# Kernel optimization log

Measured on AMD Instinct MI355X. Metric: run time of the kernel, lower is better.

Reference implementation:

```python
import jax, jax.numpy as jnp
import numpy as np

NUM_HEADS = 16
NUM_KV_HEADS = 4
HEAD_DIM = 128
BATCH = 4
SEQ = 2048  # equal per-sequence length; cu_seqlens = arange(BATCH+1)*SEQ


def setup_inputs() -> dict:
    key = jax.random.key(0)
    k1, k2, k3 = jax.random.split(key, 3)
    T = BATCH * SEQ
    q = jax.random.normal(k1, (T, NUM_HEADS * HEAD_DIM), dtype=jnp.float32)
    k = jax.random.normal(k2, (T, NUM_KV_HEADS * HEAD_DIM), dtype=jnp.float32)
    v = jax.random.normal(k3, (T, NUM_KV_HEADS * HEAD_DIM), dtype=jnp.float32)
    cu = jnp.arange(BATCH + 1, dtype=jnp.int32) * SEQ
    return {"q": q, "k": k, "v": v, "cu_seqlens_q": cu, "cu_seqlens_k": cu}


def reference(q, k, v, cu_seqlens_q, cu_seqlens_k):
    # Prefill varlen causal attention with GQA (block_tables=None path).
    # Sequences have equal length, so the ragged batch reshapes to dense [B,S,...].
    B = cu_seqlens_q.shape[0] - 1
    T = q.shape[0]
    S = T // B
    D = HEAD_DIM
    G = NUM_HEADS // NUM_KV_HEADS  # GQA group size
    qh = q.reshape(B, S, NUM_KV_HEADS, G, D)
    kh = k.reshape(B, S, NUM_KV_HEADS, D)
    vh = v.reshape(B, S, NUM_KV_HEADS, D)
    scale = 1.0 / np.sqrt(D).astype(np.float32)  # SDPA scale=None default
    # scores: [B, Hkv, G, Sq, Sk]
    scores = jnp.einsum('bqhgd,bkhd->bhgqk', qh, kh) * scale
    causal = jnp.tril(jnp.ones((S, S), dtype=bool))
    scores = jnp.where(causal, scores, jnp.finfo(scores.dtype).min)
    probs = jax.nn.softmax(scores, axis=-1)
    o = jnp.einsum('bhgqk,bkhd->bqhgd', probs, vh)
    return o.reshape(T, NUM_HEADS * HEAD_DIM)
```

## Files before the change

kernel.cpp:

```cpp
#include <hip/hip_runtime.h>


typedef __attribute__((ext_vector_type(8))) short bs8;
typedef __attribute__((ext_vector_type(16))) float f16x;
typedef __attribute__((ext_vector_type(4))) unsigned int u32x4;
typedef __attribute__((ext_vector_type(4))) unsigned short u16x4;
typedef unsigned short u16;
typedef unsigned int u32;

#define B_ 4
#define S_ 2048
#define HQ_ 16
#define HKV_ 4
#define NQT 16
#define NKT_TOT 32
#define TILE_ELEMS 8192

__device__ __forceinline__ u16 f2bf(float f) {
  u32 u = __float_as_uint(f);
  u += 0x7fffu + ((u >> 16) & 1u);
  return (u16)(u >> 16);
}

__global__ void pack_k(const float* __restrict__ k, u16* __restrict__ kp) {
  int g = blockIdx.x * 256 + threadIdx.x;
  int row = g >> 7;
  int col = (g & 127) << 2;
  int h = col >> 7, d0 = col & 127;
  int b = row >> 11, s = row & 2047;
  int kt = s >> 6, kv = s & 63;
  float4 vv = *(const float4*)(k + (size_t)row * 512 + col);
  int ti = (b * HKV_ + h) * NKT_TOT + kt;
  int e = kv * 128 + (d0 ^ (8 * (kv & 15)));
  u16x4 o;
  o.x = f2bf(vv.x); o.y = f2bf(vv.y); o.z = f2bf(vv.z); o.w = f2bf(vv.w);
  *(u16x4*)(kp + (size_t)ti * TILE_ELEMS + e) = o;
}

__global__ void pack_v(const float* __restrict__ v, u16* __restrict__ vp) {
  __shared__ u16 img[TILE_ELEMS];
  int ti = blockIdx.x;
  int kt = ti & 31;
  int bh = ti >> 5;
  int h = bh & 3, b = bh >> 2;
  int t = threadIdx.x;
#pragma unroll
  for (int p = 0; p < 8; ++p) {
    int t2 = p * 256 + t;
    int kvr = t2 >> 5;
    int d0 = (t2 & 31) << 2;
    float4 vv = *(const float4*)(v + (size_t)(b * S_ + kt * 64 + kvr) * 512 + h * 128 + d0);
    float a[4] = {vv.x, vv.y, vv.z, vv.w};
#pragma unroll
    for (int j = 0; j < 4; ++j) {
      int d = d0 + j;
      img[(d >> 1) * 128 + (d & 1) * 64 + (kvr ^ (8 * ((d >> 1) & 7)))] = f2bf(a[j]);
    }
  }
  __syncthreads();
#pragma unroll
  for (int p = 0; p < 4; ++p) {
    int e0 = (p * 256 + t) * 8;
    *(bs8*)(vp + (size_t)ti * TILE_ELEMS + e0) = *(const bs8*)&img[e0];
  }
}

__device__ __forceinline__ void gl2lds(const u16* g, u16* l) {
  __builtin_amdgcn_global_load_lds((const __attribute__((address_space(1))) void*)g,
                                   (__attribute__((address_space(3))) void*)l,
                                   16, 0, 0);
}

__global__ __launch_bounds__(256, 2) void attn_fwd(
    const float* __restrict__ q, const u16* __restrict__ kp,
    const u16* __restrict__ vp, float* __restrict__ out) {
  __shared__ u16 Ks[2][TILE_ELEMS];
  __shared__ u16 Vs[2][TILE_ELEMS];

  const int bx = blockIdx.x;
  const int qt = (NQT - 1) - (bx >> 6);
  const int bh = bx & 63;
  const int b = bh >> 4, hq = bh & 15, hkv = hq >> 2;
  const int w = threadIdx.x >> 6, lane = threadIdx.x & 63;
  const int l31 = lane & 31, hi = lane >> 5;
  const int q0 = qt * 128;
  const float scale = 0.08838834764831845f;

  bs8 qf[8];
  {
    int row = b * S_ + q0 + w * 32 + l31;
    const float* qrow = q + (size_t)row * 2048 + hq * 128;
#pragma unroll
    for (int ki = 0; ki < 8; ++ki) {
      const float* p0 = qrow + ki * 16 + hi * 8;
      float4 a = *(const float4*)p0;
      float4 c = *(const float4*)(p0 + 4);
      bs8 f;
      f[0] = (short)f2bf(a.x * scale); f[1] = (short)f2bf(a.y * scale);
      f[2] = (short)f2bf(a.z * scale); f[3] = (short)f2bf(a.w * scale);
      f[4] = (short)f2bf(c.x * scale); f[5] = (short)f2bf(c.y * scale);
      f[6] = (short)f2bf(c.z * scale); f[7] = (short)f2bf(c.w * scale);
      qf[ki] = f;
    }
  }

  f16x O[4];
#pragma unroll
  for (int dt = 0; dt < 4; ++dt)
#pragma unroll
    for (int e = 0; e < 16; ++e) O[dt][e] = 0.f;
  float m_run = -1e30f, l_run = 0.f;

  const size_t tbase = (size_t)((b * HKV_ + hkv) * NKT_TOT) * TILE_ELEMS;
  const u16* kbase = kp + tbase;
  const u16* vbase = vp + tbase;
  const int nkt = 2 * qt + 2;
  const int myrowmax = q0 + w * 32 + 31;
  const int qpos = q0 + w * 32 + l31;

  const int swzk = 8 * (l31 & 15);
  const int swzv = 8 * ((l31 >> 1) & 7);
  const int vrowbase = (l31 >> 1) * 128 + (l31 & 1) * 64;

#pragma unroll
  for (int j = 0; j < 4; ++j) {
    int c = w * 4 + j;
    gl2lds(kbase + c * 512 + lane * 8, &Ks[0][c * 512]);
    gl2lds(vbase + c * 512 + lane * 8, &Vs[0][c * 512]);
  }
  asm volatile("s_waitcnt vmcnt(0)" ::: "memory");
  __syncthreads();

  int cur = 0;
  for (int kt = 0; kt < nkt; ++kt) {
    if (kt + 1 < nkt) {
      const u16* kg = kbase + (size_t)(kt + 1) * TILE_ELEMS;
      const u16* vg = vbase + (size_t)(kt + 1) * TILE_ELEMS;
#pragma unroll
      for (int j = 0; j < 4; ++j) {
        int c = w * 4 + j;
        gl2lds(kg + c * 512 + lane * 8, &Ks[cur ^ 1][c * 512]);
        gl2lds(vg + c * 512 + lane * 8, &Vs[cur ^ 1][c * 512]);
      }
    }

    if (kt * 64 <= myrowmax) {
      f16x Sa[2];
#pragma unroll
      for (int kb = 0; kb < 2; ++kb)
#pragma unroll
        for (int e = 0; e < 16; ++e) Sa[kb][e] = 0.f;

      __builtin_amdgcn_s_setprio(1);
#pragma unroll
      for (int ki = 0; ki < 8; ++ki) {
        int koff = (ki * 16 + hi * 8) ^ swzk;
#pragma unroll
        for (int kb = 0; kb < 2; ++kb) {
          bs8 kf = *(const bs8*)&Ks[cur][(kb * 32 + l31) * 128 + koff];
          Sa[kb] = __builtin_amdgcn_mfma_f32_32x32x16_bf16(kf, qf[ki], Sa[kb], 0, 0, 0);
        }
      }
      __builtin_amdgcn_s_setprio(0);

      if (kt >= 2 * qt) {
#pragma unroll
        for (int kb = 0; kb < 2; ++kb)
#pragma unroll
          for (int r = 0; r < 16; ++r) {
            int kvpos = kt * 64 + kb * 32 + (r & 3) + 8 * (r >> 2) + 4 * hi;
            if (kvpos > qpos) Sa[kb][r] = -1e30f;
          }
      }

      float pmax = Sa[0][0];
#pragma unroll
      for (int kb = 0; kb < 2; ++kb)
#pragma unroll
        for (int r = 0; r < 16; ++r) pmax = fmaxf(pmax, Sa[kb][r]);
      pmax = fmaxf(pmax, __shfl_xor(pmax, 32, 64));

      if (__any(pmax > m_run + 8.0f)) {
        float mnew = fmaxf(m_run, pmax);
        float alpha = __expf(m_run - mnew);
        m_run = mnew;
        l_run *= alpha;
#pragma unroll
        for (int r = 0; r < 16; ++r) {
          float ar = __shfl(alpha, (r & 3) + 8 * (r >> 2) + 4 * hi, 64);
#pragma unroll
          for (int dt = 0; dt < 4; ++dt) O[dt][r] *= ar;
        }
      }

      float psum = 0.f;
#pragma unroll
      for (int kb = 0; kb < 2; ++kb)
#pragma unroll
        for (int r = 0; r < 16; ++r) {
          float p = __expf(Sa[kb][r] - m_run);
          Sa[kb][r] = p;
          psum += p;
        }
      l_run += psum;

      bs8 pf[2][2];
#pragma unroll
      for (int kb = 0; kb < 2; ++kb) {
        u32 pk_[8];
#pragma unroll
        for (int j = 0; j < 8; ++j) {
          float lo = Sa[kb][2 * j], hif = Sa[kb][2 * j + 1];
          asm("v_cvt_pk_bf16_f32 %0, %1, %2" : "=v"(pk_[j]) : "v"(lo), "v"(hif));
        }
#pragma unroll
        for (int ks = 0; ks < 2; ++ks) {
          auto s0 = __builtin_amdgcn_permlane32_swap((int)pk_[4 * ks], (int)pk_[4 * ks + 2], false, false);
          auto s1 = __builtin_amdgcn_permlane32_swap((int)pk_[4 * ks + 1], (int)pk_[4 * ks + 3], false, false);
          u32x4 fw;
          fw[0] = (u32)s0[0]; fw[1] = (u32)s1[0]; fw[2] = (u32)s0[1]; fw[3] = (u32)s1[1];
          pf[kb][ks] = __builtin_bit_cast(bs8, fw);
        }
      }

      __builtin_amdgcn_s_setprio(1);
#pragma unroll
      for (int dt = 0; dt < 4; ++dt) {
#pragma unroll
        for (int kb = 0; kb < 2; ++kb)
#pragma unroll
          for (int ks = 0; ks < 2; ++ks) {
            int kvoff = (kb * 32 + ks * 16 + hi * 8) ^ swzv;
            bs8 vb = *(const bs8*)&Vs[cur][dt * 2048 + vrowbase + kvoff];
            O[dt] = __builtin_amdgcn_mfma_f32_32x32x16_bf16(pf[kb][ks], vb, O[dt], 0, 0, 0);
          }
      }
      __builtin_amdgcn_s_setprio(0);
    }

    asm volatile("s_waitcnt vmcnt(0)" ::: "memory");
    __syncthreads();
    cur ^= 1;
  }

  float lt = l_run + __shfl_xor(l_run, 32, 64);
  float inv = 1.0f / lt;
  const int orow0 = b * S_ + q0 + w * 32;
#pragma unroll
  for (int r = 0; r < 16; ++r) {
    int qr = (r & 3) + 8 * (r >> 2) + 4 * hi;
    float li = __shfl(inv, qr, 64);
    float* op = out + (size_t)(orow0 + qr) * 2048 + hq * 128 + l31;
#pragma unroll
    for (int dt = 0; dt < 4; ++dt) op[dt * 32] = O[dt][r] * li;
  }
}

extern "C" void kernel_launch(void* const* d_in, const int* in_sizes, int n_in,
                              void* d_out, int out_size, void* d_ws, size_t ws_size,
                              hipStream_t stream) {
  const float* q = (const float*)d_in[0];
  const float* k = (const float*)d_in[1];
  const float* v = (const float*)d_in[2];
  float* out = (float*)d_out;
  u16* kp = (u16*)d_ws;
  u16* vp = kp + (size_t)B_ * HKV_ * NKT_TOT * TILE_ELEMS;

  pack_k<<<(B_ * S_ * 512 / 4) / 256, 256, 0, stream>>>(k, kp);
  pack_v<<<B_ * HKV_ * NKT_TOT, 256, 0, stream>>>(v, vp);
  attn_fwd<<<B_ * HQ_ * NQT, 256, 0, stream>>>(q, kp, vp, out);
}
```

Measured before the change: 107.9 us.

## Software-pipeline QK^T of next tile with PV of current tile, use exp2

Restructures the main loop so the QK^T MFMAs for tile t+1 are interleaved with the PV MFMAs for tile t. K is staged two tiles ahead and V one tile ahead, so softmax work can overlap with matrix-core work. It folds log2(e) into the Q scale so exp2f replaces __expf, and uses tree reductions for the row max and row sum to shorten dependency chains. The cost is more live registers (Sa kept across iterations) and a more intricate buffer-slot schedule, which could hurt occupancy at 2 blocks per CU.

```diff
diff --git a/kernel.cpp b/kernel.cpp
--- a/kernel.cpp
+++ b/kernel.cpp
@@ -84,7 +84,7 @@
   const int w = threadIdx.x >> 6, lane = threadIdx.x & 63;
   const int l31 = lane & 31, hi = lane >> 5;
   const int q0 = qt * 128;
-  const float scale = 0.08838834764831845f;
+  const float scale2 = 0.08838834764831845f * 1.4426950408889634f;
 
   bs8 qf[8];
   {
@@ -96,10 +96,10 @@
       float4 a = *(const float4*)p0;
       float4 c = *(const float4*)(p0 + 4);
       bs8 f;
-      f[0] = (short)f2bf(a.x * scale); f[1] = (short)f2bf(a.y * scale);
-      f[2] = (short)f2bf(a.z * scale); f[3] = (short)f2bf(a.w * scale);
-      f[4] = (short)f2bf(c.x * scale); f[5] = (short)f2bf(c.y * scale);
-      f[6] = (short)f2bf(c.z * scale); f[7] = (short)f2bf(c.w * scale);
+      f[0] = (short)f2bf(a.x * scale2); f[1] = (short)f2bf(a.y * scale2);
+      f[2] = (short)f2bf(a.z * scale2); f[3] = (short)f2bf(a.w * scale2);
+      f[4] = (short)f2bf(c.x * scale2); f[5] = (short)f2bf(c.y * scale2);
+      f[6] = (short)f2bf(c.z * scale2); f[7] = (short)f2bf(c.w * scale2);
       qf[ki] = f;
     }
   }
@@ -109,80 +109,86 @@
   for (int dt = 0; dt < 4; ++dt)
 #pragma unroll
     for (int e = 0; e < 16; ++e) O[dt][e] = 0.f;
+  f16x Sa[2];
   float m_run = -1e30f, l_run = 0.f;
 
   const size_t tbase = (size_t)((b * HKV_ + hkv) * NKT_TOT) * TILE_ELEMS;
   const u16* kbase = kp + tbase;
   const u16* vbase = vp + tbase;
   const int nkt = 2 * qt + 2;
-  const int myrowmax = q0 + w * 32 + 31;
+  const int L = 2 * qt + (w >> 1);
   const int qpos = q0 + w * 32 + l31;
 
   const int swzk = 8 * (l31 & 15);
   const int swzv = 8 * ((l31 >> 1) & 7);
   const int vrowbase = (l31 >> 1) * 128 + (l31 & 1) * 64;
 
-#pragma unroll
-  for (int j = 0; j < 4; ++j) {
-    int c = w * 4 + j;
-    gl2lds(kbase + c * 512 + lane * 8, &Ks[0][c * 512]);
-    gl2lds(vbase + c * 512 + lane * 8, &Vs[0][c * 512]);
-  }
+#define STAGE_K(t_, slot_)                                              \
+  {                                                                     \
+    const u16* g_ = kbase + (size_t)(t_)*TILE_ELEMS;                    \
+    _Pragma("unroll") for (int j = 0; j < 4; ++j) {                     \
+      int c = w * 4 + j;                                                \
+      gl2lds(g_ + c * 512 + lane * 8, &Ks[slot_][c * 512]);             \
+    }                                                                   \
+  }
+#define STAGE_V(t_, slot_)                                              \
+  {                                                                     \
+    const u16* g_ = vbase + (size_t)(t_)*TILE_ELEMS;                    \
+    _Pragma("unroll") for (int j = 0; j < 4; ++j) {                     \
+      int c = w * 4 + j;                                                \
+      gl2lds(g_ + c * 512 + lane * 8, &Vs[slot_][c * 512]);             \
+    }                                                                   \
+  }
+
+  STAGE_K(0, 0);
+  STAGE_V(0, 0);
+  STAGE_K(1, 1);
   asm volatile("s_waitcnt vmcnt(0)" ::: "memory");
   __syncthreads();
 
-  int cur = 0;
-  for (int kt = 0; kt < nkt; ++kt) {
-    if (kt + 1 < nkt) {
-      const u16* kg = kbase + (size_t)(kt + 1) * TILE_ELEMS;
-      const u16* vg = vbase + (size_t)(kt + 1) * TILE_ELEMS;
-#pragma unroll
-      for (int j = 0; j < 4; ++j) {
-        int c = w * 4 + j;
-        gl2lds(kg + c * 512 + lane * 8, &Ks[cur ^ 1][c * 512]);
-        gl2lds(vg + c * 512 + lane * 8, &Vs[cur ^ 1][c * 512]);
-      }
-    }
-
-    if (kt * 64 <= myrowmax) {
-      f16x Sa[2];
-#pragma unroll
-      for (int kb = 0; kb < 2; ++kb)
-#pragma unroll
-        for (int e = 0; e < 16; ++e) Sa[kb][e] = 0.f;
-
-      __builtin_amdgcn_s_setprio(1);
-#pragma unroll
-      for (int ki = 0; ki < 8; ++ki) {
-        int koff = (ki * 16 + hi * 8) ^ swzk;
-#pragma unroll
-        for (int kb = 0; kb < 2; ++kb) {
-          bs8 kf = *(const bs8*)&Ks[cur][(kb * 32 + l31) * 128 + koff];
-          Sa[kb] = __builtin_amdgcn_mfma_f32_32x32x16_bf16(kf, qf[ki], Sa[kb], 0, 0, 0);
-        }
-      }
-      __builtin_amdgcn_s_setprio(0);
-
-      if (kt >= 2 * qt) {
+#pragma unroll
+  for (int kb = 0; kb < 2; ++kb)
+#pragma unroll
+    for (int e = 0; e < 16; ++e) Sa[kb][e] = 0.f;
+#pragma unroll
+  for (int ki = 0; ki < 8; ++ki) {
+    int koff = (ki * 16 + hi * 8) ^ swzk;
+#pragma unroll
+    for (int kb = 0; kb < 2; ++kb) {
+      bs8 kf = *(const bs8*)&Ks[0][(kb * 32 + l31) * 128 + koff];
+      Sa[kb] = __builtin_amdgcn_mfma_f32_32x32x16_bf16(kf, qf[ki], Sa[kb], 0, 0, 0);
+    }
+  }
+  __syncthreads();
+
+  for (int t = 0; t < nkt; ++t) {
+    if (t + 2 < nkt) STAGE_K(t + 2, t & 1);
+    if (t + 1 < nkt) STAGE_V(t + 1, (t + 1) & 1);
+
+    bs8 pf[2][2];
+    if (t <= L) {
+      if (t >= 2 * qt) {
 #pragma unroll
         for (int kb = 0; kb < 2; ++kb)
 #pragma unroll
           for (int r = 0; r < 16; ++r) {
-            int kvpos = kt * 64 + kb * 32 + (r & 3) + 8 * (r >> 2) + 4 * hi;
+            int kvpos = t * 64 + kb * 32 + (r & 3) + 8 * (r >> 2) + 4 * hi;
             if (kvpos > qpos) Sa[kb][r] = -1e30f;
           }
       }
-
-      float pmax = Sa[0][0];
-#pragma unroll
-      for (int kb = 0; kb < 2; ++kb)
-#pragma unroll
-        for (int r = 0; r < 16; ++r) pmax = fmaxf(pmax, Sa[kb][r]);
-      pmax = fmaxf(pmax, __shfl_xor(pmax, 32, 64));
+      float tm[8];
+#pragma unroll
+      for (int r = 0; r < 8; ++r)
+        tm[r] = fmaxf(fmaxf(Sa[0][r], Sa[0][r + 8]), fmaxf(Sa[1][r], Sa[1][r + 8]));
+#pragma unroll
+      for (int s = 4; s > 0; s >>= 1)
+#pragma unroll
+        for (int r = 0; r < s; ++r) tm[r] = fmaxf(tm[r], tm[r + s]);
+      float pmax = fmaxf(tm[0], __shfl_xor(tm[0], 32, 64));
 
       if (__any(pmax > m_run + 8.0f)) {
         float mnew = fmaxf(m_run, pmax);
-        float alpha = __expf(m_run - mnew);
+        float alpha = exp2f(m_run - mnew);
         m_run = mnew;
         l_run *= alpha;
 #pragma unroll
@@ -193,18 +199,20 @@
         }
       }
 
-      float psum = 0.f;
 #pragma unroll
       for (int kb = 0; kb < 2; ++kb)
 #pragma unroll
-        for (int r = 0; r < 16; ++r) {
-          float p = __expf(Sa[kb][r] - m_run);
-          Sa[kb][r] = p;
-          psum += p;
-        }
-      l_run += psum;
-
-      bs8 pf[2][2];
+        for (int r = 0; r < 16; ++r) Sa[kb][r] = exp2f(Sa[kb][r] - m_run);
+      float ts[8];
+#pragma unroll
+      for (int r = 0; r < 8; ++r)
+        ts[r] = (Sa[0][r] + Sa[0][r + 8]) + (Sa[1][r] + Sa[1][r + 8]);
+#pragma unroll
+      for (int s = 4; s > 0; s >>= 1)
+#pragma unroll
+        for (int r = 0; r < s; ++r) ts[r] += ts[r + s];
+      l_run += ts[0];
+
 #pragma unroll
       for (int kb = 0; kb < 2; ++kb) {
         u32 pk_[8];
@@ -222,25 +230,47 @@
           pf[kb][ks] = __builtin_bit_cast(bs8, fw);
         }
       }
-
-      __builtin_amdgcn_s_setprio(1);
-#pragma unroll
-      for (int dt = 0; dt < 4; ++dt) {
+    }
+
+    __builtin_amdgcn_s_setprio(1);
+    if (t + 1 <= L) {
+#pragma unroll
+      for (int kb = 0; kb < 2; ++kb)
+#pragma unroll
+        for (int e = 0; e < 16; ++e) Sa[kb][e] = 0.f;
+#pragma unroll
+      for (int ki = 0; ki < 8; ++ki) {
+        int koff = (ki * 16 + hi * 8) ^ swzk;
+#pragma unroll
+        for (int kb = 0; kb < 2; ++kb) {
+          bs8 kf = *(const bs8*)&Ks[(t + 1) & 1][(kb * 32 + l31) * 128 + koff];
+          Sa[kb] = __builtin_amdgcn_mfma_f32_32x32x16_bf16(kf, qf[ki], Sa[kb], 0, 0, 0);
+        }
+#pragma unroll
+        for (int j = 0; j < 2; ++j) {
+          int p = 2 * ki + j;
+          int dt = p & 3, idx = p >> 2, kb = idx >> 1, ks = idx & 1;
+          int kvoff = (kb * 32 + ks * 16 + hi * 8) ^ swzv;
+          bs8 vb = *(const bs8*)&Vs[t & 1][dt * 2048 + vrowbase + kvoff];
+          O[dt] = __builtin_amdgcn_mfma_f32_32x32x16_bf16(pf[kb][ks], vb, O[dt], 0, 0, 0);
+        }
+      }
+    } else if (t <= L) {
+#pragma unroll
+      for (int dt = 0; dt < 4; ++dt)
 #pragma unroll
         for (int kb = 0; kb < 2; ++kb)
 #pragma unroll
           for (int ks = 0; ks < 2; ++ks) {
             int kvoff = (kb * 32 + ks * 16 + hi * 8) ^ swzv;
-            bs8 vb = *(const bs8*)&Vs[cur][dt * 2048 + vrowbase + kvoff];
+            bs8 vb = *(const bs8*)&Vs[t & 1][dt * 2048 + vrowbase + kvoff];
             O[dt] = __builtin_amdgcn_mfma_f32_32x32x16_bf16(pf[kb][ks], vb, O[dt], 0, 0, 0);
           }
-      }
-      __builtin_amdgcn_s_setprio(0);
-    }
+    }
+    __builtin_amdgcn_s_setprio(0);
 
     asm volatile("s_waitcnt vmcnt(0)" ::: "memory");
     __syncthreads();
-    cur ^= 1;
   }
 
   float lt = l_run + __shfl_xor(l_run, 32, 64);
```

Result: slower. 133.2 us (+23.4%).
